# Kernel tuning notes

Hardware: AMD Instinct MI355X
Metric: run time of the kernel (lower is better)

The kernel has to match this reference:

```python
import jax, jax.numpy as jnp
import numpy as np

B, N, D = 32, 20, 64          # graph pairs, max node set size, node state dim
NODE_F, EDGE_F = 16, 8        # raw feature dims
E_PER, PROP = 40, 5           # edges per graph, propagation steps
NC2 = N * (N - 1) // 2        # 190
TEMP, ITERS = 0.1, 20         # sinkhorn temperature / iterations
SRC, DST = np.triu_indices(N, 1)   # source_list / destination_list (len NC2)


def _lin(k, fin, fout):
    return jax.random.normal(k, (fin, fout), dtype=jnp.float32) / np.sqrt(fin).astype(np.float32)


def setup_inputs():
    key = jax.random.key(0)
    ks = jax.random.split(key, 24)
    tn, te = 2 * B * N, 2 * B * E_PER
    gid = jnp.repeat(jnp.arange(2 * B), E_PER)   # edges stay within their graph
    inp = {
        'node_features': jax.random.normal(ks[0], (tn, NODE_F), jnp.float32),
        'edge_features': jax.random.normal(ks[1], (te, EDGE_F), jnp.float32),
        'query_adj': (jax.random.uniform(ks[2], (B, N, N)) < 0.3).astype(jnp.float32),
        'corpus_adj': (jax.random.uniform(ks[3], (B, N, N)) < 0.3).astype(jnp.float32),
        'from_idx': jax.random.randint(ks[4], (te,), 0, N) + gid * N,
        'to_idx': jax.random.randint(ks[5], (te,), 0, N) + gid * N,
    }
    # GraphEncoder
    inp['Wn'] = _lin(ks[6], NODE_F, D); inp['bn'] = jnp.zeros(D)
    inp['We'] = _lin(ks[7], EDGE_F, D); inp['be'] = jnp.zeros(D)
    # GraphPropLayer: message net (in 3D) and node-update net (in 2D)
    inp['Wm1'] = _lin(ks[8], 3 * D, D); inp['bm1'] = jnp.zeros(D)
    inp['Wm2'] = _lin(ks[9], D, D);     inp['bm2'] = jnp.zeros(D)
    inp['Wu1'] = _lin(ks[10], 2 * D, D); inp['bu1'] = jnp.zeros(D)
    inp['Wu2'] = _lin(ks[11], D, D);     inp['bu2'] = jnp.zeros(D)
    # node_sinkhorn_feature_layers: Linear(D,N) -> ReLU -> Linear(N,N)
    inp['Ws1'] = _lin(ks[12], D, N); inp['bs1'] = jnp.zeros(N)
    inp['Ws2'] = _lin(ks[13], N, N); inp['bs2'] = jnp.zeros(N)
    # lrl_network: Linear(2D+1, D) -> ReLU -> Linear(D, D)
    inp['Wl1'] = _lin(ks[14], 2 * D + 1, D); inp['bl1'] = jnp.zeros(D)
    inp['Wl2'] = _lin(ks[15], D, D);         inp['bl2'] = jnp.zeros(D)
    return inp


def _mlp2(x, W1, b1, W2, b2):
    return jax.nn.relu(x @ W1 + b1) @ W2 + b2


def _sinkhorn(log_alpha):
    la = log_alpha / TEMP
    for _ in range(ITERS):
        la = la - jax.nn.logsumexp(la, axis=2, keepdims=True)
        la = la - jax.nn.logsumexp(la, axis=1, keepdims=True)
    return jnp.exp(la)


def _nc2_edge_emb(H, adj, Wl1, bl1, Wl2, bl2):
    s, d = H[:, SRC], H[:, DST]          # [B, NC2, D]
    e = adj[:, SRC, DST][..., None]      # [B, NC2, 1]
    fwd = _mlp2(jnp.concatenate([s, d, e], -1), Wl1, bl1, Wl2, bl2)
    bwd = _mlp2(jnp.concatenate([d, s, e], -1), Wl1, bl1, Wl2, bl2)
    return fwd + bwd


def reference(node_features, edge_features, query_adj, corpus_adj, from_idx, to_idx,
              Wn, bn, We, be, Wm1, bm1, Wm2, bm2, Wu1, bu1, Wu2, bu2,
              Ws1, bs1, Ws2, bs2, Wl1, bl1, Wl2, bl2):
    # encoder
    h = node_features @ Wn + bn
    e = edge_features @ We + be
    # GMN-style gather -> MLP -> scatter propagation
    for _ in range(PROP):
        msg = _mlp2(jnp.concatenate([h[from_idx], h[to_idx], e], -1), Wm1, bm1, Wm2, bm2)
        agg = jax.ops.segment_sum(msg, to_idx, num_segments=2 * B * N)
        h = _mlp2(jnp.concatenate([h, agg], -1), Wu1, bu1, Wu2, bu2)
    # split_and_stack (all graphs have exactly N nodes): query even, corpus odd
    H = h.reshape(2 * B, N, D)
    Hq, Hc = H[0::2], H[1::2]
    # node Sinkhorn over L1 cdist of transformed features
    Tq = _mlp2(Hq, Ws1, bs1, Ws2, bs2)
    Tc = _mlp2(Hc, Ws1, bs1, Ws2, bs2)
    cost = jnp.abs(Tq[:, :, None, :] - Tc[:, None, :, :]).sum(-1)   # [B, N, N]
    P = _sinkhorn(-cost)                                            # node transport plan
    qe = _nc2_edge_emb(Hq, query_adj, Wl1, bl1, Wl2, bl2)           # [B, NC2, D]
    ce = _nc2_edge_emb(Hc, corpus_adj, Wl1, bl1, Wl2, bl2)
    # 4-way gather-multiply edge scores: [B, NC2, NC2]
    straight = P[:, SRC[:, None], SRC[None, :]] * P[:, DST[:, None], DST[None, :]]
    cross = P[:, SRC[:, None], DST[None, :]] * P[:, DST[:, None], SRC[None, :]]
    esi = jnp.maximum(straight, cross)                              # use_max=True
    eplan = _sinkhorn(jnp.log(esi + 1e-6))                          # use_second_sinkhorn_log
    # use_m_ms_edge=True: pairwise asymmetric L1 alignment distance
    diff = qe[:, :, None, :] - ce[:, None, :, :]                    # [B, NC2, NC2, D]
    dist = (eplan * (jax.nn.relu(diff).sum(-1) + jax.nn.relu(-diff).sum(-1))).sum((-1, -2))
    return dist                                                      # [B]
```

## Files before the change

### kernel.cpp

```cpp
#include <hip/hip_runtime.h>
#include <math.h>

#define B_     32
#define N_     20
#define D_     64
#define NODE_F 16
#define EDGE_F 8
#define E_PER  40
#define PROP   5
#define NC2    190
#define ITERS  20
#define INV_TEMP 10.0f
#define TN (2*B_*N_)
#define NG (2*B_)

struct PairTab { int s[NC2]; int d[NC2]; };
constexpr PairTab make_pairs() {
    PairTab t{};
    int idx = 0;
    for (int i = 0; i < N_; ++i)
        for (int j = i + 1; j < N_; ++j) { t.s[idx] = i; t.d[idx] = j; ++idx; }
    return t;
}
__device__ constexpr PairTab PAIRS = make_pairs();

__device__ __forceinline__ float rlane(float x, int k) {
    return __int_as_float(__builtin_amdgcn_readlane(__float_as_int(x), k));
}
template<int CTRL>
__device__ __forceinline__ float dppmov(float x) {
    return __int_as_float(__builtin_amdgcn_update_dpp(
        0, __float_as_int(x), CTRL, 0xf, 0xf, false));
}
__device__ __forceinline__ float rowsum16(float x) {
    x += dppmov<0x121>(x); x += dppmov<0x122>(x);
    x += dppmov<0x124>(x); x += dppmov<0x128>(x);
    return x;
}
__device__ __forceinline__ float rowmax16(float x) {
    x = fmaxf(x, dppmov<0x121>(x)); x = fmaxf(x, dppmov<0x122>(x));
    x = fmaxf(x, dppmov<0x124>(x)); x = fmaxf(x, dppmov<0x128>(x));
    return x;
}
__device__ __forceinline__ float nrcp(float x) {
    float r = __builtin_amdgcn_rcpf(x);
    r = r * fmaf(-x, r, 2.0f);
    return r;
}

__global__ __launch_bounds__(1024, 4) void k_prop(
    const float* __restrict__ nf, const float* __restrict__ ef,
    const int* __restrict__ fidx, const int* __restrict__ tidx,
    const float* __restrict__ Wn, const float* __restrict__ bn,
    const float* __restrict__ We, const float* __restrict__ be,
    const float* __restrict__ Wm1, const float* __restrict__ bm1,
    const float* __restrict__ Wm2, const float* __restrict__ bm2,
    const float* __restrict__ Wu1, const float* __restrict__ bu1,
    const float* __restrict__ Wu2, const float* __restrict__ bu2,
    float* __restrict__ hout)
{
    __shared__ __align__(16) float wbuf[8192];
    __shared__ __align__(16) float sh[20][64];
    __shared__ __align__(16) float sE1[40][64];
    __shared__ __align__(16) float sFT[40][64];
    __shared__ __align__(16) float sa[20][64];
    __shared__ short sF[40], sD[40];
    int g = blockIdx.x, t = threadIdx.x, w = t >> 6, l = t & 63;
    int part = w >> 3, wl = w & 7;

    if (t < 40) {
        sF[t] = (short)(fidx[g * 40 + t] - g * 20);
        sD[t] = (short)(tidx[g * 40 + t] - g * 20);
    }
    for (int n = w; n < 20; n += 16) {
        float a = bn[l];
#pragma unroll
        for (int k = 0; k < NODE_F; ++k) a += nf[(g * 20 + n) * NODE_F + k] * Wn[k * 64 + l];
        sh[n][l] = a; sa[n][l] = 0.f;
    }
    {
        const float4* s4 = (const float4*)(Wm1 + 128 * 64);
        float4* d4 = (float4*)wbuf;
        if (t < 1024) d4[t] = s4[t];
    }
    __syncthreads();
    {
        int e0 = w, e1 = w + 16, e2 = w + 32;
        bool h2 = (w < 8);
        int e2c = h2 ? e2 : 0;
        float m0 = be[l], m1 = be[l], m2 = be[l];
#pragma unroll
        for (int k = 0; k < EDGE_F; ++k) {
            float wv = We[k * 64 + l];
            m0 += ef[(g * 40 + e0) * EDGE_F + k] * wv;
            m1 += ef[(g * 40 + e1) * EDGE_F + k] * wv;
            m2 += ef[(g * 40 + e2c) * EDGE_F + k] * wv;
        }
        float a0 = bm1[l], a1 = a0, a2 = a0;
#pragma unroll 4
        for (int k = 0; k < 64; ++k) {
            float wv = wbuf[k * 64 + l];
            a0 += rlane(m0, k) * wv;
            a1 += rlane(m1, k) * wv;
            a2 += rlane(m2, k) * wv;
        }
        sE1[e0][l] = a0; sE1[e1][l] = a1;
        if (h2) sE1[e2][l] = a2;
    }

    for (int step = 0; step < PROP; ++step) {
        __syncthreads();
        {
            const float4* s4 = (const float4*)Wm1;
            float4* d4 = (float4*)wbuf;
            d4[t] = s4[t]; d4[t + 1024] = s4[t + 1024];
        }
        __syncthreads();
        {
            bool h2 = (wl < 4);
            float x0 = sh[wl][l], x1 = sh[wl + 8][l];
            float x2 = h2 ? sh[wl + 16][l] : 0.f;
            float a0 = 0.f, a1 = 0.f, a2 = 0.f;
#pragma unroll 4
            for (int k = 0; k < 64; ++k) {
                float wv = wbuf[(part * 64 + k) * 64 + l];
                a0 += rlane(x0, k) * wv;
                a1 += rlane(x1, k) * wv;
                a2 += rlane(x2, k) * wv;
            }
            sFT[part * 20 + wl][l] = a0;
            sFT[part * 20 + wl + 8][l] = a1;
            if (h2) sFT[part * 20 + wl + 16][l] = a2;
        }
        __syncthreads();
        {
            const float4* s4 = (const float4*)Wm2;
            float4* d4 = (float4*)wbuf;
            if (t < 1024) d4[t] = s4[t];
        }
        __syncthreads();
        {
            bool h2 = (w < 8);
            int e0 = w, e1 = w + 16, e2c = h2 ? w + 32 : 0;
            int f0 = sF[e0], d0 = sD[e0];
            int f1 = sF[e1], d1 = sD[e1];
            int f2 = sF[e2c], d2 = sD[e2c];
            float p0 = fmaxf(sFT[f0][l] + sFT[20 + d0][l] + sE1[e0][l], 0.f);
            float p1 = fmaxf(sFT[f1][l] + sFT[20 + d1][l] + sE1[e1][l], 0.f);
            float p2 = fmaxf(sFT[f2][l] + sFT[20 + d2][l] + sE1[e2c][l], 0.f);
            float o0 = bm2[l], o1 = o0, o2 = o0;
#pragma unroll 4
            for (int k = 0; k < 64; ++k) {
                float wv = wbuf[k * 64 + l];
                o0 += rlane(p0, k) * wv;
                o1 += rlane(p1, k) * wv;
                o2 += rlane(p2, k) * wv;
            }
            atomicAdd(&sa[d0][l], o0);
            atomicAdd(&sa[d1][l], o1);
            if (h2) atomicAdd(&sa[d2][l], o2);
        }
        __syncthreads();
        {
            const float4* s4 = (const float4*)Wu1;
            float4* d4 = (float4*)wbuf;
            d4[t] = s4[t]; d4[t + 1024] = s4[t + 1024];
        }
        __syncthreads();
        {
            bool h2 = (wl < 4);
            float y0 = part ? sa[wl][l] : sh[wl][l];
            float y1 = part ? sa[wl + 8][l] : sh[wl + 8][l];
            float y2 = h2 ? (part ? sa[wl + 16][l] : sh[wl + 16][l]) : 0.f;
            float a0 = 0.f, a1 = 0.f, a2 = 0.f;
#pragma unroll 4
            for (int k = 0; k < 64; ++k) {
                float wv = wbuf[(part * 64 + k) * 64 + l];
                a0 += rlane(y0, k) * wv;
                a1 += rlane(y1, k) * wv;
                a2 += rlane(y2, k) * wv;
            }
            sFT[part * 20 + wl][l] = a0;
            sFT[part * 20 + wl + 8][l] = a1;
            if (h2) sFT[part * 20 + wl + 16][l] = a2;
        }
        __syncthreads();
        {
            const float4* s4 = (const float4*)Wu2;
            float4* d4 = (float4*)wbuf;
            if (t < 1024) d4[t] = s4[t];
        }
        __syncthreads();
        {
            bool h1 = (w < 4);
            int n0 = w, n1c = h1 ? w + 16 : 0;
            float z0 = fmaxf(sFT[n0][l] + sFT[20 + n0][l] + bu1[l], 0.f);
            float z1 = fmaxf(sFT[n1c][l] + sFT[20 + n1c][l] + bu1[l], 0.f);
            float o0 = bu2[l], o1 = o0;
#pragma unroll 4
            for (int k = 0; k < 64; ++k) {
                float wv = wbuf[k * 64 + l];
                o0 += rlane(z0, k) * wv;
                o1 += rlane(z1, k) * wv;
            }
            sh[n0][l] = o0; sa[n0][l] = 0.f;
            if (h1) { sh[n1c][l] = o1; sa[n1c][l] = 0.f; }
        }
    }
    __syncthreads();
    for (int n = w; n < 20; n += 16) hout[(g * 20 + n) * 64 + l] = sh[n][l];
}

__global__ __launch_bounds__(512, 2) void k_fuse(
    const float* __restrict__ h,
    const float* __restrict__ qadj, const float* __restrict__ cadj,
    const float* __restrict__ Ws1, const float* __restrict__ bs1,
    const float* __restrict__ Ws2, const float* __restrict__ bs2,
    const float* __restrict__ Wl1, const float* __restrict__ bl1,
    const float* __restrict__ Wl2, const float* __restrict__ bl2,
    float* __restrict__ emb, float* __restrict__ eplan, float* __restrict__ dout)
{
    __shared__ short sQs[192], sQd[192];
    __shared__ float sP[N_][N_];
    __shared__ float sVbuf[192];
    __shared__ __align__(16) float region[12288];
    int t = threadIdx.x, w = t >> 6, l = t & 63;

    if (t < 192) {
        int tt = t < NC2 ? t : NC2 - 1;
        sQs[t] = (short)PAIRS.s[tt]; sQd[t] = (short)PAIRS.d[tt];
    }
    __syncthreads();

    if (blockIdx.x < 32) {
        int b = blockIdx.x;
        if (t == 0) dout[b] = 0.f;
        float* colpart = region;
        float* sT = region + 1600;
        float* sLa = region + 2400;

        {
            int lk = (l < 20) ? l : 0;
#pragma unroll
            for (int s = 0; s < 5; ++s) {
                int r = w + 8 * s;
                float hv = h[(b * 40 + r) * 64 + l];
                float a = bs1[lk];
#pragma unroll 4
                for (int ff = 0; ff < 64; ++ff) a += rlane(hv, ff) * Ws1[ff * 20 + lk];
                a = fmaxf(a, 0.f);
                float t2 = bs2[lk];
#pragma unroll
                for (int j = 0; j < 20; ++j) t2 += rlane(a, j) * Ws2[j * 20 + lk];
                if (l < 20) sT[(r >= 20) * 400 + (r % 20) * 20 + l] = t2;
            }
        }
        __syncthreads();
        if (t < 400) {
            int i = t / 20, j = t % 20;
            float c = 0.f;
#pragma unroll
            for (int k = 0; k < 20; ++k) c += fabsf(sT[i * 20 + k] - sT[400 + j * 20 + k]);
            sLa[i * 20 + j] = -c * INV_TEMP;
        }
        __syncthreads();

        if (w == 0) {
            int q = l & 31, r2 = l >> 5;
            bool qok = (q < 20);
            float A20[10], u10[10];
#pragma unroll
            for (int i = 0; i < 10; ++i) {
                int r = 2 * i + r2;
                A20[i] = qok ? sLa[r * 20 + q] : -1e30f;
            }
            float vq = 0.f;
            for (int it = 0; it < ITERS; ++it) {
#pragma unroll
                for (int i = 0; i < 10; ++i) {
                    float x = A20[i] - vq;
                    float m = x;
#pragma unroll
                    for (int off = 16; off; off >>= 1) m = fmaxf(m, __shfl_xor(m, off));
                    float s = __expf(x - m);
#pragma unroll
                    for (int off = 16; off; off >>= 1) s += __shfl_xor(s, off);
                    u10[i] = m + __logf(s);
                }
                float pm = -1e30f;
#pragma unroll
                for (int i = 0; i < 10; ++i) pm = fmaxf(pm, A20[i] - u10[i]);
                float ps = 0.f;
#pragma unroll
                for (int i = 0; i < 10; ++i) ps += __expf(A20[i] - u10[i] - pm);
                float om = __shfl_xor(pm, 32), os = __shfl_xor(ps, 32);
                float M = fmaxf(pm, om);
                float S = ps * __expf(pm - M) + os * __expf(om - M);
                vq = M + __logf(S);
                if (!qok) vq = 0.f;
            }
#pragma unroll
            for (int i = 0; i < 10; ++i) {
                int r = 2 * i + r2;
                if (qok) sP[r][q] = __expf(A20[i] - u10[i] - vq);
            }
        }
        __syncthreads();

        int g4 = l >> 4, l16 = l & 15, rslot = w * 4 + g4;
        int sp[6], dp[6]; bool pv[6];
#pragma unroll
        for (int i = 0; i < 6; ++i) {
            int p = rslot + 32 * i;
            pv[i] = (p < NC2);
            int pc = pv[i] ? p : 0;
            sp[i] = sQs[pc]; dp[i] = sQd[pc];
        }
        int sq[12], dq[12]; bool qv[12];
#pragma unroll
        for (int j = 0; j < 12; ++j) {
            int q = l16 + 16 * j;
            qv[j] = (q < NC2);
            int qc = qv[j] ? q : 0;
            sq[j] = sQs[qc]; dq[j] = sQd[qc];
        }

        float AE[6][12];
#pragma unroll
        for (int i = 0; i < 6; ++i)
#pragma unroll
            for (int j = 0; j < 12; ++j) {
                if (pv[i] && qv[j]) {
                    float st = sP[sp[i]][sq[j]] * sP[dp[i]][dq[j]];
                    float cr = sP[sp[i]][dq[j]] * sP[dp[i]][sq[j]];
                    AE[i][j] = __logf(fmaxf(st, cr) + 1e-6f) * INV_TEMP;
                } else AE[i][j] = -1e30f;
            }

        float u[6];
#pragma unroll
        for (int i = 0; i < 6; ++i) {
            float m = -1e30f;
#pragma unroll
            for (int j = 0; j < 12; ++j) m = fmaxf(m, AE[i][j]);
            m = rowmax16(m);
            float s = 0.f;
#pragma unroll
            for (int j = 0; j < 12; ++j) s += __expf(AE[i][j] - m);
            s = rowsum16(s);
            u[i] = m + __logf(s);
            if (!pv[i]) u[i] = 0.f;
        }
#pragma unroll
        for (int j = 0; j < 12; ++j) {
            float pm = -1e30f;
#pragma unroll
            for (int i = 0; i < 6; ++i) if (pv[i]) pm = fmaxf(pm, AE[i][j] - u[i]);
            pm = fmaxf(pm, __shfl_xor(pm, 16));
            pm = fmaxf(pm, __shfl_xor(pm, 32));
            if (g4 == 0) colpart[w * 200 + l16 + 16 * j] = pm;
        }
        __syncthreads();
        if (t < 192) {
            float M = -1e30f;
#pragma unroll
            for (int s = 0; s < 8; ++s) M = fmaxf(M, colpart[s * 200 + t]);
            sVbuf[t] = M;
        }
        __syncthreads();
        float Mj[12];
#pragma unroll
        for (int j = 0; j < 12; ++j) Mj[j] = sVbuf[l16 + 16 * j];
#pragma unroll
        for (int j = 0; j < 12; ++j) {
            float ps = 0.f;
#pragma unroll
            for (int i = 0; i < 6; ++i) if (pv[i]) ps += __expf(AE[i][j] - u[i] - Mj[j]);
            ps += __shfl_xor(ps, 16);
            ps += __shfl_xor(ps, 32);
            if (g4 == 0) colpart[w * 200 + l16 + 16 * j] = ps;
        }
        __syncthreads();
        if (t < 192) {
            float S = 0.f;
#pragma unroll
            for (int s = 0; s < 8; ++s) S += colpart[s * 200 + t];
            sVbuf[t] = sVbuf[t] + __logf(fmaxf(S, 1e-37f));
        }
        __syncthreads();
#pragma unroll
        for (int j = 0; j < 12; ++j) Mj[j] = sVbuf[l16 + 16 * j];
#pragma unroll
        for (int i = 0; i < 6; ++i)
#pragma unroll
            for (int j = 0; j < 12; ++j) {
                float e = __expf(AE[i][j] - u[i] - Mj[j]);
                AE[i][j] = (pv[i] && qv[j]) ? e : 0.f;
            }
        __syncthreads();

        float invS[6];
        for (int it = 0; it < ITERS - 1; ++it) {
#pragma unroll
            for (int i = 0; i < 6; ++i) {
                float s01 = AE[i][0] + AE[i][1], s23 = AE[i][2] + AE[i][3];
                float s45 = AE[i][4] + AE[i][5], s67 = AE[i][6] + AE[i][7];
                float s89 = AE[i][8] + AE[i][9], sab = AE[i][10] + AE[i][11];
                float S = ((s01 + s23) + (s45 + s67)) + (s89 + sab);
                S = rowsum16(S);
                invS[i] = nrcp(fmaxf(S, 1e-30f));
            }
#pragma unroll
            for (int j = 0; j < 12; ++j) {
                float pc = AE[0][j] * invS[0];
                pc = fmaf(AE[1][j], invS[1], pc);
                pc = fmaf(AE[2][j], invS[2], pc);
                pc = fmaf(AE[3][j], invS[3], pc);
                pc = fmaf(AE[4][j], invS[4], pc);
                pc = fmaf(AE[5][j], invS[5], pc);
                pc += __shfl_xor(pc, 16);
                pc += __shfl_xor(pc, 32);
                if (g4 == 0) colpart[w * 200 + l16 + 16 * j] = pc;
            }
            __syncthreads();
            if (t < 192) {
                float c = 0.f;
#pragma unroll
                for (int s = 0; s < 8; ++s) c += colpart[s * 200 + t];
                sVbuf[t] = nrcp(fmaxf(c, 1e-30f));
            }
            __syncthreads();
            float ic[12];
#pragma unroll
            for (int j = 0; j < 12; ++j) ic[j] = sVbuf[l16 + 16 * j];
#pragma unroll
            for (int i = 0; i < 6; ++i)
#pragma unroll
                for (int j = 0; j < 12; ++j) {
                    float tmp = AE[i][j] * invS[i];
                    AE[i][j] = tmp * ic[j];
                }
        }

        float* ep = eplan + (size_t)b * NC2 * NC2;
#pragma unroll
        for (int i = 0; i < 6; ++i) {
            if (pv[i]) {
                int p = rslot + 32 * i;
                float* row = ep + (size_t)p * NC2;
#pragma unroll
                for (int j = 0; j < 12; ++j)
                    if (qv[j]) row[l16 + 16 * j] = AE[i][j];
            }
        }
    } else {
        int eb = blockIdx.x - 32;
        float* wb1 = region;
        float* wb2 = region + 8192;
        {
            const float4* s1 = (const float4*)Wl1;
            float4* d1 = (float4*)wb1;
#pragma unroll
            for (int i = 0; i < 4; ++i) d1[t + 512 * i] = s1[t + 512 * i];
            const float4* s2 = (const float4*)Wl2;
            float4* d2 = (float4*)wb2;
#pragma unroll
            for (int i = 0; i < 2; ++i) d2[t + 512 * i] = s2[t + 512 * i];
        }
        float b1 = bl1[l];
        float w128 = Wl1[128 * 64 + l];
        float b2 = 2.f * bl2[l];
        __syncthreads();

        int base = eb * 48 + w * 6;
        float sv[6], dv[6], av[6]; bool val[6]; int gi[6], pp[6];
#pragma unroll
        for (int s = 0; s < 6; ++s) {
            int sid = base + s;
            val[s] = (sid < NG * NC2);
            int sc = val[s] ? sid : 0;
            gi[s] = sc / NC2;
            pp[s] = sc - gi[s] * NC2;
            int bb = gi[s] >> 1, gg = gi[s] & 1;
            int spi = sQs[pp[s]], dpi = sQd[pp[s]];
            sv[s] = h[(bb * 40 + gg * 20 + spi) * 64 + l];
            dv[s] = h[(bb * 40 + gg * 20 + dpi) * 64 + l];
            const float* adj = gg ? cadj : qadj;
            av[s] = adj[bb * 400 + spi * 20 + dpi];
        }
        float aF[6], aB[6];
#pragma unroll
        for (int s = 0; s < 6; ++s) { float t0 = b1 + av[s] * w128; aF[s] = t0; aB[s] = t0; }
#pragma unroll 2
        for (int k = 0; k < 64; ++k) {
            float w0 = wb1[k * 64 + l];
            float w1 = wb1[(64 + k) * 64 + l];
#pragma unroll
            for (int s = 0; s < 6; ++s) {
                float a = rlane(sv[s], k), c = rlane(dv[s], k);
                aF[s] += a * w0 + c * w1;
                aB[s] += c * w0 + a * w1;
            }
        }
        float hs[6], out[6];
#pragma unroll
        for (int s = 0; s < 6; ++s) { hs[s] = fmaxf(aF[s], 0.f) + fmaxf(aB[s], 0.f); out[s] = b2; }
#pragma unroll 4
        for (int k = 0; k < 64; ++k) {
            float ww = wb2[k * 64 + l];
#pragma unroll
            for (int s = 0; s < 6; ++s) out[s] += rlane(hs[s], k) * ww;
        }
#pragma unroll
        for (int s = 0; s < 6; ++s)
            if (val[s]) emb[((size_t)gi[s] * NC2 + pp[s]) * 64 + l] = out[s];
    }
}

__global__ __launch_bounds__(256) void k_dist(
    const float* __restrict__ emb, const float* __restrict__ eplan, float* __restrict__ dout)
{
    int b = blockIdx.x, c = blockIdx.y;
    int w = threadIdx.x >> 6, l = threadIdx.x & 63;
    const float* qe = emb + (size_t)(2 * b) * NC2 * D_;
    const float* ce = emb + (size_t)(2 * b + 1) * NC2 * D_;
    const float* W = eplan + (size_t)b * NC2 * NC2;
    float acc = 0.f;
    int pbase = c * 16 + w * 4;
    for (int i = 0; i < 4; ++i) {
        int p = pbase + i;
        if (p >= NC2) break;
        float qv = qe[(size_t)p * D_ + l];
        const float* wrow = W + (size_t)p * NC2;
        for (int q = 0; q < NC2; ++q)
            acc += wrow[q] * fabsf(qv - ce[(size_t)q * D_ + l]);
    }
#pragma unroll
    for (int off = 32; off; off >>= 1) acc += __shfl_xor(acc, off);
    if (l == 0) atomicAdd(&dout[b], acc);
}

extern "C" void kernel_launch(void* const* d_in, const int* in_sizes, int n_in,
                              void* d_out, int out_size, void* d_ws, size_t ws_size,
                              hipStream_t stream)
{
    const float* nf   = (const float*)d_in[0];
    const float* ef   = (const float*)d_in[1];
    const float* qadj = (const float*)d_in[2];
    const float* cadj = (const float*)d_in[3];
    const int*   fidx = (const int*)d_in[4];
    const int*   tidx = (const int*)d_in[5];
    const float* Wn  = (const float*)d_in[6];  const float* bn  = (const float*)d_in[7];
    const float* We  = (const float*)d_in[8];  const float* be  = (const float*)d_in[9];
    const float* Wm1 = (const float*)d_in[10]; const float* bm1 = (const float*)d_in[11];
    const float* Wm2 = (const float*)d_in[12]; const float* bm2 = (const float*)d_in[13];
    const float* Wu1 = (const float*)d_in[14]; const float* bu1 = (const float*)d_in[15];
    const float* Wu2 = (const float*)d_in[16]; const float* bu2 = (const float*)d_in[17];
    const float* Ws1 = (const float*)d_in[18]; const float* bs1 = (const float*)d_in[19];
    const float* Ws2 = (const float*)d_in[20]; const float* bs2 = (const float*)d_in[21];
    const float* Wl1 = (const float*)d_in[22]; const float* bl1 = (const float*)d_in[23];
    const float* Wl2 = (const float*)d_in[24]; const float* bl2 = (const float*)d_in[25];

    float* ws    = (float*)d_ws;
    float* h     = ws;
    float* emb   = h + (size_t)TN * 64;
    float* eplan = emb + (size_t)NG * NC2 * 64;
    float* dout  = (float*)d_out;

    k_prop<<<NG, 1024, 0, stream>>>(nf, ef, fidx, tidx, Wn, bn, We, be,
                                    Wm1, bm1, Wm2, bm2, Wu1, bu1, Wu2, bu2, h);
    k_fuse<<<32 + 254, 512, 0, stream>>>(h, qadj, cadj, Ws1, bs1, Ws2, bs2,
                                         Wl1, bl1, Wl2, bl2, emb, eplan, dout);
    k_dist<<<dim3(B_, 12), 256, 0, stream>>>(emb, eplan, dout);
}
```

Baseline: 357.7 us.

## Split fused kernel into edge-embedding and 1024-thread Sinkhorn kernels

```diff
diff --git a/kernel.cpp b/kernel.cpp
--- a/kernel.cpp
+++ b/kernel.cpp
@@ -211,39 +211,33 @@
     for (int n = w; n < 20; n += 16) hout[(g * 20 + n) * 64 + l] = sh[n][l];
 }
 
-__global__ __launch_bounds__(512, 2) void k_fuse(
+__global__ __launch_bounds__(1024) void k_simsink(
     const float* __restrict__ h,
-    const float* __restrict__ qadj, const float* __restrict__ cadj,
     const float* __restrict__ Ws1, const float* __restrict__ bs1,
     const float* __restrict__ Ws2, const float* __restrict__ bs2,
-    const float* __restrict__ Wl1, const float* __restrict__ bl1,
-    const float* __restrict__ Wl2, const float* __restrict__ bl2,
-    float* __restrict__ emb, float* __restrict__ eplan, float* __restrict__ dout)
+    float* __restrict__ eplan, float* __restrict__ dout)
 {
     __shared__ short sQs[192], sQd[192];
     __shared__ float sP[N_][N_];
     __shared__ float sVbuf[192];
-    __shared__ __align__(16) float region[12288];
-    int t = threadIdx.x, w = t >> 6, l = t & 63;
+    __shared__ __align__(16) float region[3400];
+    int b = blockIdx.x, t = threadIdx.x, w = t >> 6, l = t & 63;
 
     if (t < 192) {
         int tt = t < NC2 ? t : NC2 - 1;
         sQs[t] = (short)PAIRS.s[tt]; sQd[t] = (short)PAIRS.d[tt];
     }
-    __syncthreads();
-
-    if (blockIdx.x < 32) {
-        int b = blockIdx.x;
-        if (t == 0) dout[b] = 0.f;
-        float* colpart = region;
-        float* sT = region + 1600;
-        float* sLa = region + 2400;
-
-        {
-            int lk = (l < 20) ? l : 0;
-#pragma unroll
-            for (int s = 0; s < 5; ++s) {
-                int r = w + 8 * s;
+    if (t == 0) dout[b] = 0.f;
+    float* sT = region;
+    float* sLa = region + 800;
+    float* colpart = region;
+
+    {
+        int lk = (l < 20) ? l : 0;
+#pragma unroll
+        for (int s = 0; s < 3; ++s) {
+            int r = w + 16 * s;
+            if (r < 40) {
                 float hv = h[(b * 40 + r) * 64 + l];
                 float a = bs1[lk];
 #pragma unroll 4
@@ -255,266 +249,272 @@
                 if (l < 20) sT[(r >= 20) * 400 + (r % 20) * 20 + l] = t2;
             }
         }
-        __syncthreads();
-        if (t < 400) {
-            int i = t / 20, j = t % 20;
-            float c = 0.f;
-#pragma unroll
-            for (int k = 0; k < 20; ++k) c += fabsf(sT[i * 20 + k] - sT[400 + j * 20 + k]);
-            sLa[i * 20 + j] = -c * INV_TEMP;
-        }
-        __syncthreads();
-
-        if (w == 0) {
-            int q = l & 31, r2 = l >> 5;
-            bool qok = (q < 20);
-            float A20[10], u10[10];
+    }
+    __syncthreads();
+    if (t < 400) {
+        int i = t / 20, j = t % 20;
+        float c = 0.f;
+#pragma unroll
+        for (int k = 0; k < 20; ++k) c += fabsf(sT[i * 20 + k] - sT[400 + j * 20 + k]);
+        sLa[i * 20 + j] = -c * INV_TEMP;
+    }
+    __syncthreads();
+
+    if (w == 0) {
+        int q = l & 31, r2 = l >> 5;
+        bool qok = (q < 20);
+        float A20[10], u10[10];
+#pragma unroll
+        for (int i = 0; i < 10; ++i) {
+            int r = 2 * i + r2;
+            A20[i] = qok ? sLa[r * 20 + q] : -1e30f;
+        }
+        float vq = 0.f;
+        for (int it = 0; it < ITERS; ++it) {
 #pragma unroll
             for (int i = 0; i < 10; ++i) {
-                int r = 2 * i + r2;
-                A20[i] = qok ? sLa[r * 20 + q] : -1e30f;
+                float x = A20[i] - vq;
+                float m = x;
+#pragma unroll
+                for (int off = 16; off; off >>= 1) m = fmaxf(m, __shfl_xor(m, off));
+                float s = __expf(x - m);
+#pragma unroll
+                for (int off = 16; off; off >>= 1) s += __shfl_xor(s, off);
+                u10[i] = m + __logf(s);
             }
-            float vq = 0.f;
-            for (int it = 0; it < ITERS; ++it) {
-#pragma unroll
-                for (int i = 0; i < 10; ++i) {
-                    float x = A20[i] - vq;
-                    float m = x;
-#pragma unroll
-                    for (int off = 16; off; off >>= 1) m = fmaxf(m, __shfl_xor(m, off));
-                    float s = __expf(x - m);
-#pragma unroll
-                    for (int off = 16; off; off >>= 1) s += __shfl_xor(s, off);
-                    u10[i] = m + __logf(s);
-                }
-                float pm = -1e30f;
-#pragma unroll
-                for (int i = 0; i < 10; ++i) pm = fmaxf(pm, A20[i] - u10[i]);
-                float ps = 0.f;
-#pragma unroll
-                for (int i = 0; i < 10; ++i) ps += __expf(A20[i] - u10[i] - pm);
-                float om = __shfl_xor(pm, 32), os = __shfl_xor(ps, 32);
-                float M = fmaxf(pm, om);
-                float S = ps * __expf(pm - M) + os * __expf(om - M);
-                vq = M + __logf(S);
-                if (!qok) vq = 0.f;
-            }
-#pragma unroll
-            for (int i = 0; i < 10; ++i) {
-                int r = 2 * i + r2;
-                if (qok) sP[r][q] = __expf(A20[i] - u10[i] - vq);
-            }
-        }
-        __syncthreads();
-
-        int g4 = l >> 4, l16 = l & 15, rslot = w * 4 + g4;
-        int sp[6], dp[6]; bool pv[6];
-#pragma unroll
-        for (int i = 0; i < 6; ++i) {
-            int p = rslot + 32 * i;
-            pv[i] = (p < NC2);
-            int pc = pv[i] ? p : 0;
-            sp[i] = sQs[pc]; dp[i] = sQd[pc];
-        }
-        int sq[12], dq[12]; bool qv[12];
+            float pm = -1e30f;
+#pragma unroll
+            for (int i = 0; i < 10; ++i) pm = fmaxf(pm, A20[i] - u10[i]);
+            float ps = 0.f;
+#pragma unroll
+            for (int i = 0; i < 10; ++i) ps += __expf(A20[i] - u10[i] - pm);
+            float om = __shfl_xor(pm, 32), os = __shfl_xor(ps, 32);
+            float M = fmaxf(pm, om);
+            float S = ps * __expf(pm - M) + os * __expf(om - M);
+            vq = M + __logf(S);
+            if (!qok) vq = 0.f;
+        }
+#pragma unroll
+        for (int i = 0; i < 10; ++i) {
+            int r = 2 * i + r2;
+            if (qok) sP[r][q] = __expf(A20[i] - u10[i] - vq);
+        }
+    }
+    __syncthreads();
+
+    int g4 = l >> 4, l16 = l & 15, rslot = w * 4 + g4;
+    int sp[3], dp[3]; bool pv[3];
+#pragma unroll
+    for (int i = 0; i < 3; ++i) {
+        int p = rslot + 64 * i;
+        pv[i] = (p < NC2);
+        int pc = pv[i] ? p : 0;
+        sp[i] = sQs[pc]; dp[i] = sQd[pc];
+    }
+    int sq[12], dq[12]; bool qv[12];
+#pragma unroll
+    for (int j = 0; j < 12; ++j) {
+        int q = l16 + 16 * j;
+        qv[j] = (q < NC2);
+        int qc = qv[j] ? q : 0;
+        sq[j] = sQs[qc]; dq[j] = sQd[qc];
+    }
+
+    float AE[3][12];
+#pragma unroll
+    for (int i = 0; i < 3; ++i)
 #pragma unroll
         for (int j = 0; j < 12; ++j) {
-            int q = l16 + 16 * j;
-            qv[j] = (q < NC2);
-            int qc = qv[j] ? q : 0;
-            sq[j] = sQs[qc]; dq[j] = sQd[qc];
-        }
-
-        float AE[6][12];
-#pragma unroll
-        for (int i = 0; i < 6; ++i)
-#pragma unroll
-            for (int j = 0; j < 12; ++j) {
-                if (pv[i] && qv[j]) {
-                    float st = sP[sp[i]][sq[j]] * sP[dp[i]][dq[j]];
-                    float cr = sP[sp[i]][dq[j]] * sP[dp[i]][sq[j]];
-                    AE[i][j] = __logf(fmaxf(st, cr) + 1e-6f) * INV_TEMP;
-                } else AE[i][j] = -1e30f;
-            }
-
-        float u[6];
-#pragma unroll
-        for (int i = 0; i < 6; ++i) {
-            float m = -1e30f;
-#pragma unroll
-            for (int j = 0; j < 12; ++j) m = fmaxf(m, AE[i][j]);
-            m = rowmax16(m);
-            float s = 0.f;
-#pragma unroll
-            for (int j = 0; j < 12; ++j) s += __expf(AE[i][j] - m);
-            s = rowsum16(s);
-            u[i] = m + __logf(s);
-            if (!pv[i]) u[i] = 0.f;
-        }
+            if (pv[i] && qv[j]) {
+                float st = sP[sp[i]][sq[j]] * sP[dp[i]][dq[j]];
+                float cr = sP[sp[i]][dq[j]] * sP[dp[i]][sq[j]];
+                AE[i][j] = __logf(fmaxf(st, cr) + 1e-6f) * INV_TEMP;
+            } else AE[i][j] = -1e30f;
+        }
+
+    float u[3];
+#pragma unroll
+    for (int i = 0; i < 3; ++i) {
+        float m = -1e30f;
+#pragma unroll
+        for (int j = 0; j < 12; ++j) m = fmaxf(m, AE[i][j]);
+        m = rowmax16(m);
+        float s = 0.f;
+#pragma unroll
+        for (int j = 0; j < 12; ++j) s += __expf(AE[i][j] - m);
+        s = rowsum16(s);
+        u[i] = m + __logf(s);
+        if (!pv[i]) u[i] = 0.f;
+    }
+#pragma unroll
+    for (int j = 0; j < 12; ++j) {
+        float pm = -1e30f;
+#pragma unroll
+        for (int i = 0; i < 3; ++i) if (pv[i]) pm = fmaxf(pm, AE[i][j] - u[i]);
+        pm = fmaxf(pm, __shfl_xor(pm, 16));
+        pm = fmaxf(pm, __shfl_xor(pm, 32));
+        if (g4 == 0) colpart[w * 200 + l16 + 16 * j] = pm;
+    }
+    __syncthreads();
+    if (t < 192) {
+        float M = -1e30f;
+#pragma unroll
+        for (int s = 0; s < 16; ++s) M = fmaxf(M, colpart[s * 200 + t]);
+        sVbuf[t] = M;
+    }
+    __syncthreads();
+    float cj[12];
+#pragma unroll
+    for (int j = 0; j < 12; ++j) cj[j] = sVbuf[l16 + 16 * j];
+#pragma unroll
+    for (int j = 0; j < 12; ++j) {
+        float ps = 0.f;
+#pragma unroll
+        for (int i = 0; i < 3; ++i) if (pv[i]) ps += __expf(AE[i][j] - u[i] - cj[j]);
+        ps += __shfl_xor(ps, 16);
+        ps += __shfl_xor(ps, 32);
+        if (g4 == 0) colpart[w * 200 + l16 + 16 * j] = ps;
+    }
+    __syncthreads();
+    if (t < 192) {
+        float S = 0.f;
+#pragma unroll
+        for (int s = 0; s < 16; ++s) S += colpart[s * 200 + t];
+        sVbuf[t] = sVbuf[t] + __logf(fmaxf(S, 1e-37f));
+    }
+    __syncthreads();
+#pragma unroll
+    for (int j = 0; j < 12; ++j) cj[j] = sVbuf[l16 + 16 * j];
+#pragma unroll
+    for (int i = 0; i < 3; ++i)
 #pragma unroll
         for (int j = 0; j < 12; ++j) {
-            float pm = -1e30f;
-#pragma unroll
-            for (int i = 0; i < 6; ++i) if (pv[i]) pm = fmaxf(pm, AE[i][j] - u[i]);
-            pm = fmaxf(pm, __shfl_xor(pm, 16));
-            pm = fmaxf(pm, __shfl_xor(pm, 32));
-            if (g4 == 0) colpart[w * 200 + l16 + 16 * j] = pm;
+            float e = __expf(AE[i][j] - u[i] - cj[j]);
+            AE[i][j] = (pv[i] && qv[j]) ? e : 0.f;
+        }
+    __syncthreads();
+
+    float r[3];
+#pragma unroll
+    for (int j = 0; j < 12; ++j) cj[j] = 1.f;
+    for (int it = 0; it < ITERS - 1; ++it) {
+#pragma unroll
+        for (int i = 0; i < 3; ++i) {
+            float S = AE[i][0] * cj[0];
+#pragma unroll
+            for (int j = 1; j < 12; ++j) S = fmaf(AE[i][j], cj[j], S);
+            S = rowsum16(S);
+            r[i] = nrcp(fmaxf(S, 1e-30f));
+        }
+#pragma unroll
+        for (int j = 0; j < 12; ++j) {
+            float pc = AE[0][j] * r[0];
+            pc = fmaf(AE[1][j], r[1], pc);
+            pc = fmaf(AE[2][j], r[2], pc);
+            pc += __shfl_xor(pc, 16);
+            pc += __shfl_xor(pc, 32);
+            if (g4 == 0) colpart[w * 200 + l16 + 16 * j] = pc;
         }
         __syncthreads();
         if (t < 192) {
-            float M = -1e30f;
-#pragma unroll
-            for (int s = 0; s < 8; ++s) M = fmaxf(M, colpart[s * 200 + t]);
-            sVbuf[t] = M;
-        }
-        __syncthreads();
-        float Mj[12];
-#pragma unroll
-        for (int j = 0; j < 12; ++j) Mj[j] = sVbuf[l16 + 16 * j];
-#pragma unroll
-        for (int j = 0; j < 12; ++j) {
-            float ps = 0.f;
-#pragma unroll
-            for (int i = 0; i < 6; ++i) if (pv[i]) ps += __expf(AE[i][j] - u[i] - Mj[j]);
-            ps += __shfl_xor(ps, 16);
-            ps += __shfl_xor(ps, 32);
-            if (g4 == 0) colpart[w * 200 + l16 + 16 * j] = ps;
-        }
-        __syncthreads();
-        if (t < 192) {
-            float S = 0.f;
-#pragma unroll
-            for (int s = 0; s < 8; ++s) S += colpart[s * 200 + t];
-            sVbuf[t] = sVbuf[t] + __logf(fmaxf(S, 1e-37f));
-        }
-        __syncthreads();
-#pragma unroll
-        for (int j = 0; j < 12; ++j) Mj[j] = sVbuf[l16 + 16 * j];
-#pragma unroll
-        for (int i = 0; i < 6; ++i)
-#pragma unroll
-            for (int j = 0; j < 12; ++j) {
-                float e = __expf(AE[i][j] - u[i] - Mj[j]);
-                AE[i][j] = (pv[i] && qv[j]) ? e : 0.f;
-            }
-        __syncthreads();
-
-        float invS[6];
-        for (int it = 0; it < ITERS - 1; ++it) {
-#pragma unroll
-            for (int i = 0; i < 6; ++i) {
-                float s01 = AE[i][0] + AE[i][1], s23 = AE[i][2] + AE[i][3];
-                float s45 = AE[i][4] + AE[i][5], s67 = AE[i][6] + AE[i][7];
-                float s89 = AE[i][8] + AE[i][9], sab = AE[i][10] + AE[i][11];
-                float S = ((s01 + s23) + (s45 + s67)) + (s89 + sab);
-                S = rowsum16(S);
-                invS[i] = nrcp(fmaxf(S, 1e-30f));
-            }
-#pragma unroll
-            for (int j = 0; j < 12; ++j) {
-                float pc = AE[0][j] * invS[0];
-                pc = fmaf(AE[1][j], invS[1], pc);
-                pc = fmaf(AE[2][j], invS[2], pc);
-                pc = fmaf(AE[3][j], invS[3], pc);
-                pc = fmaf(AE[4][j], invS[4], pc);
-                pc = fmaf(AE[5][j], invS[5], pc);
-                pc += __shfl_xor(pc, 16);
-                pc += __shfl_xor(pc, 32);
-                if (g4 == 0) colpart[w * 200 + l16 + 16 * j] = pc;
-            }
-            __syncthreads();
-            if (t < 192) {
-                float c = 0.f;
-#pragma unroll
-                for (int s = 0; s < 8; ++s) c += colpart[s * 200 + t];
-                sVbuf[t] = nrcp(fmaxf(c, 1e-30f));
-            }
-            __syncthreads();
-            float ic[12];
-#pragma unroll
-            for (int j = 0; j < 12; ++j) ic[j] = sVbuf[l16 + 16 * j];
-#pragma unroll
-            for (int i = 0; i < 6; ++i)
-#pragma unroll
-                for (int j = 0; j < 12; ++j) {
-                    float tmp = AE[i][j] * invS[i];
-                    AE[i][j] = tmp * ic[j];
-                }
-        }
-
-        float* ep = eplan + (size_t)b * NC2 * NC2;
-#pragma unroll
-        for (int i = 0; i < 6; ++i) {
-            if (pv[i]) {
-                int p = rslot + 32 * i;
-                float* row = ep + (size_t)p * NC2;
-#pragma unroll
-                for (int j = 0; j < 12; ++j)
-                    if (qv[j]) row[l16 + 16 * j] = AE[i][j];
-            }
-        }
-    } else {
-        int eb = blockIdx.x - 32;
-        float* wb1 = region;
-        float* wb2 = region + 8192;
-        {
-            const float4* s1 = (const float4*)Wl1;
-            float4* d1 = (float4*)wb1;
-#pragma unroll
-            for (int i = 0; i < 4; ++i) d1[t + 512 * i] = s1[t + 512 * i];
-            const float4* s2 = (const float4*)Wl2;
-            float4* d2 = (float4*)wb2;
-#pragma unroll
-            for (int i = 0; i < 2; ++i) d2[t + 512 * i] = s2[t + 512 * i];
-        }
-        float b1 = bl1[l];
-        float w128 = Wl1[128 * 64 + l];
-        float b2 = 2.f * bl2[l];
-        __syncthreads();
-
-        int base = eb * 48 + w * 6;
-        float sv[6], dv[6], av[6]; bool val[6]; int gi[6], pp[6];
+            float C = 0.f;
+#pragma unroll
+            for (int s = 0; s < 16; ++s) C += colpart[s * 200 + t];
+            sVbuf[t] = nrcp(fmaxf(C, 1e-30f));
+        }
+        __syncthreads();
+#pragma unroll
+        for (int j = 0; j < 12; ++j) cj[j] = sVbuf[l16 + 16 * j];
+    }
+
+    float* ep = eplan + (size_t)b * NC2 * NC2;
+#pragma unroll
+    for (int i = 0; i < 3; ++i) {
+        if (pv[i]) {
+            int p = rslot + 64 * i;
+            float* row = ep + (size_t)p * NC2;
+#pragma unroll
+            for (int j = 0; j < 12; ++j)
+                if (qv[j]) row[l16 + 16 * j] = AE[i][j] * r[i] * cj[j];
+        }
+    }
+}
+
+__global__ __launch_bounds__(512) void k_edge(
+    const float* __restrict__ h,
+    const float* __restrict__ qadj, const float* __restrict__ cadj,
+    const float* __restrict__ Wl1, const float* __restrict__ bl1,
+    const float* __restrict__ Wl2, const float* __restrict__ bl2,
+    float* __restrict__ emb)
+{
+    __shared__ short sQs[192], sQd[192];
+    __shared__ __align__(16) float wbuf[12288];
+    int t = threadIdx.x, w = t >> 6, l = t & 63;
+    int eb = blockIdx.x;
+
+    if (t < 192) {
+        int tt = t < NC2 ? t : NC2 - 1;
+        sQs[t] = (short)PAIRS.s[tt]; sQd[t] = (short)PAIRS.d[tt];
+    }
+    float* wb1 = wbuf;
+    float* wb2 = wbuf + 8192;
+    {
+        const float4* s1 = (const float4*)Wl1;
+        float4* d1 = (float4*)wb1;
+#pragma unroll
+        for (int i = 0; i < 4; ++i) d1[t + 512 * i] = s1[t + 512 * i];
+        const float4* s2 = (const float4*)Wl2;
+        float4* d2 = (float4*)wb2;
+#pragma unroll
+        for (int i = 0; i < 2; ++i) d2[t + 512 * i] = s2[t + 512 * i];
+    }
+    float b1 = bl1[l];
+    float w128 = Wl1[128 * 64 + l];
+    float b2 = 2.f * bl2[l];
+    __syncthreads();
+
+    int base = eb * 48 + w * 6;
+    float sv[6], dv[6], av[6]; bool val[6]; int gi[6], pp[6];
+#pragma unroll
+    for (int s = 0; s < 6; ++s) {
+        int sid = base + s;
+        val[s] = (sid < NG * NC2);
+        int sc = val[s] ? sid : 0;
+        gi[s] = sc / NC2;
+        pp[s] = sc - gi[s] * NC2;
+        int bb = gi[s] >> 1, gg = gi[s] & 1;
+        int spi = sQs[pp[s]], dpi = sQd[pp[s]];
+        sv[s] = h[(bb * 40 + gg * 20 + spi) * 64 + l];
+        dv[s] = h[(bb * 40 + gg * 20 + dpi) * 64 + l];
+        const float* adj = gg ? cadj : qadj;
+        av[s] = adj[bb * 400 + spi * 20 + dpi];
+    }
+    float aF[6], aB[6];
+#pragma unroll
+    for (int s = 0; s < 6; ++s) { float t0 = b1 + av[s] * w128; aF[s] = t0; aB[s] = t0; }
+#pragma unroll 2
+    for (int k = 0; k < 64; ++k) {
+        float w0 = wb1[k * 64 + l];
+        float w1 = wb1[(64 + k) * 64 + l];
 #pragma unroll
         for (int s = 0; s < 6; ++s) {
-            int sid = base + s;
-            val[s] = (sid < NG * NC2);
-            int sc = val[s] ? sid : 0;
-            gi[s] = sc / NC2;
-            pp[s] = sc - gi[s] * NC2;
-            int bb = gi[s] >> 1, gg = gi[s] & 1;
-            int spi = sQs[pp[s]], dpi = sQd[pp[s]];
-            sv[s] = h[(bb * 40 + gg * 20 + spi) * 64 + l];
-            dv[s] = h[(bb * 40 + gg * 20 + dpi) * 64 + l];
-            const float* adj = gg ? cadj : qadj;
-            av[s] = adj[bb * 400 + spi * 20 + dpi];
-        }
-        float aF[6], aB[6];
-#pragma unroll
-        for (int s = 0; s < 6; ++s) { float t0 = b1 + av[s] * w128; aF[s] = t0; aB[s] = t0; }
-#pragma unroll 2
-        for (int k = 0; k < 64; ++k) {
-            float w0 = wb1[k * 64 + l];
-            float w1 = wb1[(64 + k) * 64 + l];
-#pragma unroll
-            for (int s = 0; s < 6; ++s) {
-                float a = rlane(sv[s], k), c = rlane(dv[s], k);
-                aF[s] += a * w0 + c * w1;
-                aB[s] += c * w0 + a * w1;
-            }
-        }
-        float hs[6], out[6];
-#pragma unroll
-        for (int s = 0; s < 6; ++s) { hs[s] = fmaxf(aF[s], 0.f) + fmaxf(aB[s], 0.f); out[s] = b2; }
-#pragma unroll 4
-        for (int k = 0; k < 64; ++k) {
-            float ww = wb2[k * 64 + l];
-#pragma unroll
-            for (int s = 0; s < 6; ++s) out[s] += rlane(hs[s], k) * ww;
-        }
-#pragma unroll
-        for (int s = 0; s < 6; ++s)
-            if (val[s]) emb[((size_t)gi[s] * NC2 + pp[s]) * 64 + l] = out[s];
-    }
+            float a = rlane(sv[s], k), c = rlane(dv[s], k);
+            aF[s] += a * w0 + c * w1;
+            aB[s] += c * w0 + a * w1;
+        }
+    }
+    float hs[6], out[6];
+#pragma unroll
+    for (int s = 0; s < 6; ++s) { hs[s] = fmaxf(aF[s], 0.f) + fmaxf(aB[s], 0.f); out[s] = b2; }
+#pragma unroll 4
+    for (int k = 0; k < 64; ++k) {
+        float ww = wb2[k * 64 + l];
+#pragma unroll
+        for (int s = 0; s < 6; ++s) out[s] += rlane(hs[s], k) * ww;
+    }
+#pragma unroll
+    for (int s = 0; s < 6; ++s)
+        if (val[s]) emb[((size_t)gi[s] * NC2 + pp[s]) * 64 + l] = out[s];
 }
 
 __global__ __launch_bounds__(256) void k_dist(
@@ -569,7 +569,7 @@
 
     k_prop<<<NG, 1024, 0, stream>>>(nf, ef, fidx, tidx, Wn, bn, We, be,
                                     Wm1, bm1, Wm2, bm2, Wu1, bu1, Wu2, bu2, h);
-    k_fuse<<<32 + 254, 512, 0, stream>>>(h, qadj, cadj, Ws1, bs1, Ws2, bs2,
-                                         Wl1, bl1, Wl2, bl2, emb, eplan, dout);
+    k_edge<<<254, 512, 0, stream>>>(h, qadj, cadj, Wl1, bl1, Wl2, bl2, emb);
+    k_simsink<<<B_, 1024, 0, stream>>>(h, Ws1, bs1, Ws2, bs2, eplan, dout);
     k_dist<<<dim3(B_, 12), 256, 0, stream>>>(emb, eplan, dout);
 }
```

New measurement: 371.5 us. 1.04x slower.
